# Kernel tuning notes

Measured on AMD Instinct MI355X. Metric: run time of the kernel, lower is better.

Reference implementation:

```python
import jax, jax.numpy as jnp
import numpy as np

B, C, H, W = 4, 32, 512, 512


def _warp_add(x, flow, residual):
    # x: [B,C,H,W], flow: [B,2,H,W], residual: [B,C,H,W]
    Bs, Cs, Hs, Ws = x.shape
    # align_corners=False pixel-center base grid in [-1,1]
    gy = (jnp.arange(Hs, dtype=x.dtype) + 0.5) * (2.0 / Hs) - 1.0  # [H]
    gx = (jnp.arange(Ws, dtype=x.dtype) + 0.5) * (2.0 / Ws) - 1.0  # [W]
    grid_x = gx[None, None, :] + flow[:, 0]  # [B,H,W]
    grid_y = gy[None, :, None] + flow[:, 1]  # [B,H,W]
    # circular wrap on x only
    grid_x = jnp.mod(grid_x + 1.0, 2.0) - 1.0
    real_x = (grid_x + 1.0) * (Ws * 0.5) - 0.5
    real_y = (grid_y + 1.0) * (Hs * 0.5) - 0.5
    x0 = jnp.floor(real_x)
    y0 = jnp.floor(real_y)
    dx = real_x - x0
    dy = real_y - y0
    ix0 = x0.astype(jnp.int32)
    iy0 = y0.astype(jnp.int32)
    ix1 = ix0 + 1
    iy1 = iy0 + 1

    def valid(ix, iy):
        return (ix >= 0) & (ix < Ws) & (iy >= 0) & (iy < Hs)

    xf = x.reshape(Bs, Cs, Hs * Ws)

    def gather(ix, iy):
        v = valid(ix, iy)  # [B,H,W]
        idx = jnp.clip(iy, 0, Hs - 1) * Ws + jnp.clip(ix, 0, Ws - 1)  # [B,H,W]
        g = jnp.take_along_axis(xf, idx.reshape(Bs, 1, Hs * Ws), axis=2)  # [B,C,H*W]
        g = g.reshape(Bs, Cs, Hs, Ws)
        return jnp.where(v[:, None, :, :], g, 0.0)

    v_tl = gather(ix0, iy0)
    v_tr = gather(ix1, iy0)
    v_bl = gather(ix0, iy1)
    v_br = gather(ix1, iy1)

    w_tl = ((1.0 - dx) * (1.0 - dy))[:, None]
    w_tr = (dx * (1.0 - dy))[:, None]
    w_bl = ((1.0 - dx) * dy)[:, None]
    w_br = (dx * dy)[:, None]

    out = w_tl * v_tl + w_tr * v_tr + w_bl * v_bl + w_br * v_br + residual
    return out


def setup_inputs() -> dict:
    key = jax.random.key(0)
    k1, k2, k3 = jax.random.split(key, 3)
    x = jax.random.normal(k1, (B, C, H, W), dtype=jnp.float32)
    flow = jax.random.normal(k2, (B, 2, H, W), dtype=jnp.float32) * 0.1
    residual = jax.random.normal(k3, (B, C, H, W), dtype=jnp.float32)
    return {"x": x, "flow": flow, "residual": residual}


def reference(x, flow, residual):
    return _warp_add(x, flow, residual)
```

## Files before the change

kernel.cpp:

```cpp
#include <hip/hip_runtime.h>

#define Bdim 4
#define Cdim 32
#define Hdim 512
#define Wdim 512
#define HWdim (Hdim * Wdim)

typedef __attribute__((ext_vector_type(4))) float    f32x4;
typedef __attribute__((ext_vector_type(2))) _Float16 f16x2;
typedef __attribute__((ext_vector_type(4))) _Float16 f16x4;
typedef __attribute__((ext_vector_type(8))) _Float16 f16x8;

__global__ __launch_bounds__(256) void transpose_nhwc_half_kernel(
    const float* __restrict__ x, _Float16* __restrict__ ws)
{
    __shared__ float lds[Cdim * 132];

    const int idx = blockIdx.x;
    const int tw  = idx & 3;
    const int h   = (idx >> 2) & (Hdim - 1);
    const int b   = idx >> 11;
    const int w0  = tw * 128;
    const int t   = threadIdx.x;

    f32x4 r[4];
    #pragma unroll
    for (int i = 0; i < 4; ++i) {
        const int f4 = i * 256 + t;
        const int c  = f4 >> 5;
        const int w4 = f4 & 31;
        r[i] = *(const f32x4*)(x + (((size_t)b * Cdim + c) * Hdim + h) * Wdim + w0 + w4 * 4);
    }
    #pragma unroll
    for (int i = 0; i < 4; ++i) {
        const int f4 = i * 256 + t;
        *(f32x4*)(lds + (f4 >> 5) * 132 + (f4 & 31) * 4) = r[i];
    }
    __syncthreads();

    const size_t base = (((size_t)b * Hdim + h) * Wdim + w0) * Cdim;
    const int w_ = t >> 1;
    const int c0 = (t & 1) * 16;
    f16x8 v0, v1;
    #pragma unroll
    for (int k = 0; k < 8; ++k) v0[k] = (_Float16)lds[(c0 + k) * 132 + w_];
    #pragma unroll
    for (int k = 0; k < 8; ++k) v1[k] = (_Float16)lds[(c0 + 8 + k) * 132 + w_];
    *(f16x8*)(ws + base + (size_t)w_ * Cdim + c0)     = v0;
    *(f16x8*)(ws + base + (size_t)w_ * Cdim + c0 + 8) = v1;
}

__global__ __launch_bounds__(256) void gather_nhwc_half_kernel(
    const _Float16* __restrict__ ws,
    const float* __restrict__ flow,
    const float* __restrict__ residual,
    float* __restrict__ out)
{
    __shared__ int      s_off[4][256];
    __shared__ float    s_wt[4][256];
    __shared__ _Float16 s_buf[128 * 34];

    const int idx = blockIdx.x;
    const int b   = idx >> 10;
    const int h   = (idx >> 1) & (Hdim - 1);
    const int w0  = (idx & 1) << 8;
    const int t   = threadIdx.x;

    {
        const int w = w0 + t;
        const int pixg = h * Wdim + w;
        const float fx = flow[((size_t)b * 2 + 0) * HWdim + pixg];
        const float fy = flow[((size_t)b * 2 + 1) * HWdim + pixg];

        float gx = ((float)w + 0.5f) * (2.0f / (float)Wdim) - 1.0f + fx;
        float gy = ((float)h + 0.5f) * (2.0f / (float)Hdim) - 1.0f + fy;

        float tm = fmodf(gx + 1.0f, 2.0f);
        if (tm < 0.0f) tm += 2.0f;
        gx = tm - 1.0f;

        const float real_x = (gx + 1.0f) * ((float)Wdim * 0.5f) - 0.5f;
        const float real_y = (gy + 1.0f) * ((float)Hdim * 0.5f) - 0.5f;

        const float x0f = floorf(real_x);
        const float y0f = floorf(real_y);
        const float dx = real_x - x0f;
        const float dy = real_y - y0f;

        const int ix0 = (int)x0f;
        const int iy0 = (int)y0f;
        const int ix1 = ix0 + 1;
        const int iy1 = iy0 + 1;

        const bool vx0 = (ix0 >= 0) && (ix0 < Wdim);
        const bool vx1 = (ix1 >= 0) && (ix1 < Wdim);
        const bool vy0 = (iy0 >= 0) && (iy0 < Hdim);
        const bool vy1 = (iy1 >= 0) && (iy1 < Hdim);

        const int cx0 = min(max(ix0, 0), Wdim - 1);
        const int cx1 = min(max(ix1, 0), Wdim - 1);
        const int cy0 = min(max(iy0, 0), Hdim - 1);
        const int cy1 = min(max(iy1, 0), Hdim - 1);

        float w_tl = (1.0f - dx) * (1.0f - dy);
        float w_tr = dx * (1.0f - dy);
        float w_bl = (1.0f - dx) * dy;
        float w_br = dx * dy;
        if (!(vx0 && vy0)) w_tl = 0.0f;
        if (!(vx1 && vy0)) w_tr = 0.0f;
        if (!(vx0 && vy1)) w_bl = 0.0f;
        if (!(vx1 && vy1)) w_br = 0.0f;

        s_off[0][t] = (cy0 * Wdim + cx0) * Cdim;
        s_off[1][t] = (cy0 * Wdim + cx1) * Cdim;
        s_off[2][t] = (cy1 * Wdim + cx0) * Cdim;
        s_off[3][t] = (cy1 * Wdim + cx1) * Cdim;
        s_wt[0][t] = w_tl;
        s_wt[1][t] = w_tr;
        s_wt[2][t] = w_bl;
        s_wt[3][t] = w_br;
    }
    __syncthreads();

    const int ci = t & 7;
    const int c0 = ci * 4;
    const int p  = t >> 3;
    const _Float16* xb = ws + (size_t)b * (size_t)HWdim * Cdim + c0;

    #pragma unroll
    for (int half = 0; half < 2; ++half) {
        #pragma unroll 4
        for (int j = 0; j < 4; ++j) {
            const int lpix = j * 32 + p;
            const int pix  = half * 128 + lpix;
            const int o0 = s_off[0][pix];
            const int o1 = s_off[1][pix];
            const int o2 = s_off[2][pix];
            const int o3 = s_off[3][pix];
            const float w0_ = s_wt[0][pix];
            const float w1_ = s_wt[1][pix];
            const float w2_ = s_wt[2][pix];
            const float w3_ = s_wt[3][pix];

            const f16x4 v0 = *(const f16x4*)(xb + o0);
            const f16x4 v1 = *(const f16x4*)(xb + o1);
            const f16x4 v2 = *(const f16x4*)(xb + o2);
            const f16x4 v3 = *(const f16x4*)(xb + o3);

            float a0 = w0_ * (float)v0[0] + w1_ * (float)v1[0] + w2_ * (float)v2[0] + w3_ * (float)v3[0];
            float a1 = w0_ * (float)v0[1] + w1_ * (float)v1[1] + w2_ * (float)v2[1] + w3_ * (float)v3[1];
            float a2 = w0_ * (float)v0[2] + w1_ * (float)v1[2] + w2_ * (float)v2[2] + w3_ * (float)v3[2];
            float a3 = w0_ * (float)v0[3] + w1_ * (float)v1[3] + w2_ * (float)v2[3] + w3_ * (float)v3[3];

            f16x2 h01; h01[0] = (_Float16)a0; h01[1] = (_Float16)a1;
            f16x2 h23; h23[0] = (_Float16)a2; h23[1] = (_Float16)a3;
            *(f16x2*)(s_buf + lpix * 34 + c0)     = h01;
            *(f16x2*)(s_buf + lpix * 34 + c0 + 2) = h23;
        }
        __syncthreads();

        {
            const int lpix = t >> 1;
            const int ch0  = (t & 1) * 16;
            const size_t pbase = (size_t)h * Wdim + w0 + half * 128 + lpix;
            const _Float16* row = s_buf + lpix * 34 + ch0;
            #pragma unroll 8
            for (int cc = 0; cc < 16; cc += 2) {
                const f16x2 v = *(const f16x2*)(row + cc);
                const size_t gi0 = ((size_t)b * Cdim + ch0 + cc) * HWdim + pbase;
                const float r0 = __builtin_nontemporal_load(residual + gi0);
                const float r1 = __builtin_nontemporal_load(residual + gi0 + HWdim);
                __builtin_nontemporal_store((float)v[0] + r0, out + gi0);
                __builtin_nontemporal_store((float)v[1] + r1, out + gi0 + HWdim);
            }
        }
        if (half == 0) __syncthreads();
    }
}

__global__ __launch_bounds__(256) void warp_add_kernel(
    const float* __restrict__ x,
    const float* __restrict__ flow,
    const float* __restrict__ residual,
    float* __restrict__ out)
{
    int tid = blockIdx.x * blockDim.x + threadIdx.x;
    int w = tid & (Wdim - 1);
    int h = (tid >> 9) & (Hdim - 1);
    int b = tid >> 18;

    const float fx = flow[((size_t)b * 2 + 0) * HWdim + h * Wdim + w];
    const float fy = flow[((size_t)b * 2 + 1) * HWdim + h * Wdim + w];

    float gx = ((float)w + 0.5f) * (2.0f / (float)Wdim) - 1.0f + fx;
    float gy = ((float)h + 0.5f) * (2.0f / (float)Hdim) - 1.0f + fy;
    {
        float t2 = fmodf(gx + 1.0f, 2.0f);
        if (t2 < 0.0f) t2 += 2.0f;
        gx = t2 - 1.0f;
    }
    const float real_x = (gx + 1.0f) * ((float)Wdim * 0.5f) - 0.5f;
    const float real_y = (gy + 1.0f) * ((float)Hdim * 0.5f) - 0.5f;
    const float x0f = floorf(real_x);
    const float y0f = floorf(real_y);
    const float dx = real_x - x0f;
    const float dy = real_y - y0f;
    const int ix0 = (int)x0f, iy0 = (int)y0f;
    const int ix1 = ix0 + 1,  iy1 = iy0 + 1;
    const bool vx0 = (ix0 >= 0) && (ix0 < Wdim);
    const bool vx1 = (ix1 >= 0) && (ix1 < Wdim);
    const bool vy0 = (iy0 >= 0) && (iy0 < Hdim);
    const bool vy1 = (iy1 >= 0) && (iy1 < Hdim);
    const int cx0 = min(max(ix0, 0), Wdim - 1);
    const int cx1 = min(max(ix1, 0), Wdim - 1);
    const int cy0 = min(max(iy0, 0), Hdim - 1);
    const int cy1 = min(max(iy1, 0), Hdim - 1);
    float w_tl = (1.0f - dx) * (1.0f - dy);
    float w_tr = dx * (1.0f - dy);
    float w_bl = (1.0f - dx) * dy;
    float w_br = dx * dy;
    if (!(vx0 && vy0)) w_tl = 0.0f;
    if (!(vx1 && vy0)) w_tr = 0.0f;
    if (!(vx0 && vy1)) w_bl = 0.0f;
    if (!(vx1 && vy1)) w_br = 0.0f;
    const int off_tl = cy0 * Wdim + cx0;
    const int off_tr = cy0 * Wdim + cx1;
    const int off_bl = cy1 * Wdim + cx0;
    const int off_br = cy1 * Wdim + cx1;
    const size_t base = (size_t)b * Cdim * HWdim;
    const int    pix  = h * Wdim + w;
    const float* xb = x + base;
    const float* rbp = residual + base + pix;
    float*       ob = out + base + pix;
    #pragma unroll 8
    for (int c = 0; c < Cdim; ++c) {
        const float* xc = xb + (size_t)c * HWdim;
        float v = w_tl * xc[off_tl] + w_tr * xc[off_tr]
                + w_bl * xc[off_bl] + w_br * xc[off_br]
                + rbp[(size_t)c * HWdim];
        ob[(size_t)c * HWdim] = v;
    }
}

extern "C" void kernel_launch(void* const* d_in, const int* in_sizes, int n_in,
                              void* d_out, int out_size, void* d_ws, size_t ws_size,
                              hipStream_t stream) {
    const float* x        = (const float*)d_in[0];
    const float* flow     = (const float*)d_in[1];
    const float* residual = (const float*)d_in[2];
    float* out            = (float*)d_out;

    const size_t ws_needed = (size_t)Bdim * Cdim * HWdim * sizeof(_Float16);

    if (ws_size >= ws_needed) {
        _Float16* ws = (_Float16*)d_ws;
        transpose_nhwc_half_kernel<<<Bdim * Hdim * (Wdim / 128), 256, 0, stream>>>(x, ws);
        gather_nhwc_half_kernel<<<Bdim * Hdim * Wdim / 256, 256, 0, stream>>>(ws, flow, residual, out);
    } else {
        const int total = Bdim * Hdim * Wdim;
        warp_add_kernel<<<total / 256, 256, 0, stream>>>(x, flow, residual, out);
    }
}
```

Baseline: 354.7 us.

## Make gather kernel wave-local with shuffles, prefetch, and swizzled block order

Replaces the shared-memory offset/weight tables and block-wide barriers with per-wave processing: each wave fetches its own pixels' offsets and weights through cross-lane shuffles, software-pipelines the four corner loads one iteration ahead, and stages results in a per-wave LDS slice using only a wave barrier. Blocks are also remapped in an interleaved order to change which rows run concurrently and improve locality in the cache. The intent is to remove __syncthreads stalls and hide gather latency, at the cost of more registers and a dependence on wave-level LDS ordering.

```diff
diff --git a/kernel.cpp b/kernel.cpp
--- a/kernel.cpp
+++ b/kernel.cpp
@@ -56,16 +56,20 @@
     const float* __restrict__ residual,
     float* __restrict__ out)
 {
-    __shared__ int      s_off[4][256];
-    __shared__ float    s_wt[4][256];
-    __shared__ _Float16 s_buf[128 * 34];
-
-    const int idx = blockIdx.x;
-    const int b   = idx >> 10;
-    const int h   = (idx >> 1) & (Hdim - 1);
-    const int w0  = (idx & 1) << 8;
-    const int t   = threadIdx.x;
-
+    __shared__ _Float16 s_buf[4 * 64 * 34];
+
+    const int orig = blockIdx.x;
+    const int idx  = (orig & 7) * 512 + (orig >> 3);
+
+    const int b    = idx >> 10;
+    const int h    = (idx >> 1) & (Hdim - 1);
+    const int w0   = (idx & 1) << 8;
+    const int t    = threadIdx.x;
+    const int lane = t & 63;
+    const int wv   = t >> 6;
+
+    int   off0, off1, off2, off3;
+    float wt0,  wt1,  wt2,  wt3;
     {
         const int w = w0 + t;
         const int pixg = h * Wdim + w;
@@ -111,70 +115,82 @@
         if (!(vx0 && vy1)) w_bl = 0.0f;
         if (!(vx1 && vy1)) w_br = 0.0f;
 
-        s_off[0][t] = (cy0 * Wdim + cx0) * Cdim;
-        s_off[1][t] = (cy0 * Wdim + cx1) * Cdim;
-        s_off[2][t] = (cy1 * Wdim + cx0) * Cdim;
-        s_off[3][t] = (cy1 * Wdim + cx1) * Cdim;
-        s_wt[0][t] = w_tl;
-        s_wt[1][t] = w_tr;
-        s_wt[2][t] = w_bl;
-        s_wt[3][t] = w_br;
-    }
-    __syncthreads();
-
-    const int ci = t & 7;
-    const int c0 = ci * 4;
-    const int p  = t >> 3;
-    const _Float16* xb = ws + (size_t)b * (size_t)HWdim * Cdim + c0;
-
-    #pragma unroll
-    for (int half = 0; half < 2; ++half) {
-        #pragma unroll 4
-        for (int j = 0; j < 4; ++j) {
-            const int lpix = j * 32 + p;
-            const int pix  = half * 128 + lpix;
-            const int o0 = s_off[0][pix];
-            const int o1 = s_off[1][pix];
-            const int o2 = s_off[2][pix];
-            const int o3 = s_off[3][pix];
-            const float w0_ = s_wt[0][pix];
-            const float w1_ = s_wt[1][pix];
-            const float w2_ = s_wt[2][pix];
-            const float w3_ = s_wt[3][pix];
-
-            const f16x4 v0 = *(const f16x4*)(xb + o0);
-            const f16x4 v1 = *(const f16x4*)(xb + o1);
-            const f16x4 v2 = *(const f16x4*)(xb + o2);
-            const f16x4 v3 = *(const f16x4*)(xb + o3);
-
-            float a0 = w0_ * (float)v0[0] + w1_ * (float)v1[0] + w2_ * (float)v2[0] + w3_ * (float)v3[0];
-            float a1 = w0_ * (float)v0[1] + w1_ * (float)v1[1] + w2_ * (float)v2[1] + w3_ * (float)v3[1];
-            float a2 = w0_ * (float)v0[2] + w1_ * (float)v1[2] + w2_ * (float)v2[2] + w3_ * (float)v3[2];
-            float a3 = w0_ * (float)v0[3] + w1_ * (float)v1[3] + w2_ * (float)v2[3] + w3_ * (float)v3[3];
+        off0 = (cy0 * Wdim + cx0) * Cdim;
+        off1 = (cy0 * Wdim + cx1) * Cdim;
+        off2 = (cy1 * Wdim + cx0) * Cdim;
+        off3 = (cy1 * Wdim + cx1) * Cdim;
+        wt0 = w_tl; wt1 = w_tr; wt2 = w_bl; wt3 = w_br;
+    }
+
+    {
+        const int ci = lane & 7;
+        const int c0 = ci * 4;
+        const int ps = lane >> 3;
+        const _Float16* xb = ws + (size_t)b * (size_t)HWdim * Cdim + c0;
+        _Float16* sb = s_buf + wv * (64 * 34);
+
+        int   co[4]; float cw[4]; f16x4 cv[4];
+        {
+            const int sj = ps;
+            co[0] = __shfl(off0, sj, 64); co[1] = __shfl(off1, sj, 64);
+            co[2] = __shfl(off2, sj, 64); co[3] = __shfl(off3, sj, 64);
+            cw[0] = __shfl(wt0, sj, 64);  cw[1] = __shfl(wt1, sj, 64);
+            cw[2] = __shfl(wt2, sj, 64);  cw[3] = __shfl(wt3, sj, 64);
+            #pragma unroll
+            for (int k = 0; k < 4; ++k) cv[k] = *(const f16x4*)(xb + co[k]);
+        }
+
+        #pragma unroll
+        for (int j = 0; j < 8; ++j) {
+            int   no[4]; float nw[4]; f16x4 nv[4];
+            if (j < 7) {
+                const int sj = (j + 1) * 8 + ps;
+                no[0] = __shfl(off0, sj, 64); no[1] = __shfl(off1, sj, 64);
+                no[2] = __shfl(off2, sj, 64); no[3] = __shfl(off3, sj, 64);
+                nw[0] = __shfl(wt0, sj, 64);  nw[1] = __shfl(wt1, sj, 64);
+                nw[2] = __shfl(wt2, sj, 64);  nw[3] = __shfl(wt3, sj, 64);
+                #pragma unroll
+                for (int k = 0; k < 4; ++k) nv[k] = *(const f16x4*)(xb + no[k]);
+            }
+
+            const int lpix = j * 8 + ps;
+            const float a0 = cw[0] * (float)cv[0][0] + cw[1] * (float)cv[1][0]
+                           + cw[2] * (float)cv[2][0] + cw[3] * (float)cv[3][0];
+            const float a1 = cw[0] * (float)cv[0][1] + cw[1] * (float)cv[1][1]
+                           + cw[2] * (float)cv[2][1] + cw[3] * (float)cv[3][1];
+            const float a2 = cw[0] * (float)cv[0][2] + cw[1] * (float)cv[1][2]
+                           + cw[2] * (float)cv[2][2] + cw[3] * (float)cv[3][2];
+            const float a3 = cw[0] * (float)cv[0][3] + cw[1] * (float)cv[1][3]
+                           + cw[2] * (float)cv[2][3] + cw[3] * (float)cv[3][3];
 
             f16x2 h01; h01[0] = (_Float16)a0; h01[1] = (_Float16)a1;
             f16x2 h23; h23[0] = (_Float16)a2; h23[1] = (_Float16)a3;
-            *(f16x2*)(s_buf + lpix * 34 + c0)     = h01;
-            *(f16x2*)(s_buf + lpix * 34 + c0 + 2) = h23;
-        }
-        __syncthreads();
-
-        {
-            const int lpix = t >> 1;
-            const int ch0  = (t & 1) * 16;
-            const size_t pbase = (size_t)h * Wdim + w0 + half * 128 + lpix;
-            const _Float16* row = s_buf + lpix * 34 + ch0;
-            #pragma unroll 8
-            for (int cc = 0; cc < 16; cc += 2) {
-                const f16x2 v = *(const f16x2*)(row + cc);
-                const size_t gi0 = ((size_t)b * Cdim + ch0 + cc) * HWdim + pbase;
-                const float r0 = __builtin_nontemporal_load(residual + gi0);
-                const float r1 = __builtin_nontemporal_load(residual + gi0 + HWdim);
-                __builtin_nontemporal_store((float)v[0] + r0, out + gi0);
-                __builtin_nontemporal_store((float)v[1] + r1, out + gi0 + HWdim);
+            *(f16x2*)(sb + lpix * 34 + c0)     = h01;
+            *(f16x2*)(sb + lpix * 34 + c0 + 2) = h23;
+
+            if (j < 7) {
+                #pragma unroll
+                for (int k = 0; k < 4; ++k) { co[k] = no[k]; cw[k] = nw[k]; cv[k] = nv[k]; }
             }
         }
-        if (half == 0) __syncthreads();
+    }
+
+    __builtin_amdgcn_wave_barrier();
+    asm volatile("s_waitcnt lgkmcnt(0)" ::: "memory");
+    __builtin_amdgcn_sched_barrier(0);
+
+    {
+        const size_t pbase = (size_t)h * Wdim + w0 + t;
+        const _Float16* row = s_buf + wv * (64 * 34) + lane * 34;
+        #pragma unroll 8
+        for (int cc = 0; cc < Cdim; cc += 2) {
+            const f16x2 v = *(const f16x2*)(row + cc);
+            const size_t gi0 = ((size_t)b * Cdim + cc) * HWdim + pbase;
+            const float r0 = __builtin_nontemporal_load(residual + gi0);
+            const float r1 = __builtin_nontemporal_load(residual + gi0 + HWdim);
+            __builtin_nontemporal_store((float)v[0] + r0, out + gi0);
+            __builtin_nontemporal_store((float)v[1] + r1, out + gi0 + HWdim);
+        }
     }
 }
 
```

After: 344.1 us. -3.0%, faster.
